# Kernel tuning notes

Measured on AMD Instinct MI355X. Metric: run time of the kernel, lower is better.

Reference implementation:

```python
import jax, jax.numpy as jnp
import numpy as np

N_HEAD = 12
MIN_SIZE = 4
MAX_SIZE = 8
TOP_M = 16
ALPHA = 1.0
EPS = 1e-6
NEG_INF = -1e30


def setup_inputs() -> dict:
    key = jax.random.key(0)
    ks = jax.random.split(key, 4)
    B, T, C = 2, 512, 768
    x = jax.random.normal(ks[0], (B, T, C), jnp.float32)
    w_qkv = jax.random.normal(ks[1], (C, 3 * C), jnp.float32) * (1.0 / np.sqrt(C))
    b_qkv = jnp.zeros((3 * C,), jnp.float32)
    w_proj = jax.random.normal(ks[2], (C, C), jnp.float32) * (1.0 / np.sqrt(C))
    b_proj = jnp.zeros((C,), jnp.float32)
    gate_param = jnp.zeros((), jnp.float32)  # dpp_gate_init = 0.0 -> gate = 0.5
    return {"x": x, "w_qkv": w_qkv, "b_qkv": b_qkv, "w_proj": w_proj,
            "b_proj": b_proj, "gate_param": gate_param}


def _dpp_token(i, q_i, k, v):
    """Greedy DPP subset selection + attention for one query token.
    q_i: [hd], k/v: [T, hd]. Faithful to the torch greedy loop, vectorized
    over candidates with incremental Gram construction (scores only gate the
    discrete selection, so they are computed under stop_gradient, matching
    torch where they only feed Python comparisons)."""
    T, hd = k.shape
    kc = jax.lax.stop_gradient(k)
    qc = jax.lax.stop_gradient(q_i)
    # causal similarity, topk candidates
    sim = jnp.where(jnp.arange(T) <= i, kc @ qc, NEG_INF)
    _, topidx = jax.lax.top_k(sim, TOP_M)  # [M]
    # candidates = top-min(TOP_M, i+1) causal neighbors, excluding i itself
    cand_active = (jnp.arange(TOP_M) < jnp.minimum(TOP_M, i + 1)) & (topidx != i)
    cand_keys = kc[topidx]                              # [M, hd]
    cnorm = jnp.sum(cand_keys * cand_keys, axis=-1)     # [M]

    sel_idx = jnp.zeros((MAX_SIZE,), jnp.int32).at[0].set(i)
    sel_count = jnp.int32(1)
    # initial score: log(det([k_i.k_i]) + eps) / 1**alpha
    cur = jnp.log(jnp.dot(kc[i], kc[i]) + EPS)
    stopped = jnp.bool_(False)
    eye = jnp.eye(MAX_SIZE, dtype=jnp.float32)
    slots = jnp.arange(MAX_SIZE)

    for _ in range(MAX_SIZE - 1):
        rowmask = slots < sel_count                       # [S] current subset rows
        pos = (slots == sel_count).astype(jnp.float32)    # slot for new candidate
        Ksel = kc[sel_idx] * rowmask[:, None].astype(jnp.float32)  # [S, hd]
        G0 = Ksel @ Ksel.T                                # [S, S]
        cross = cand_keys @ Ksel.T                        # [M, S]
        # Gc[c,a,b] = G0[a,b] + pos[a]*cross[c,b] + pos[b]*cross[c,a] + pos[a]pos[b]*cnorm[c]
        Gc = (G0[None]
              + pos[None, :, None] * cross[:, None, :]
              + pos[None, None, :] * cross[:, :, None]
              + (pos[:, None] * pos[None, :])[None] * cnorm[:, None, None])
        newmask = rowmask | (slots == sel_count)
        # identity-pad unused rows/cols so det equals det of the active submatrix
        Gc = Gc + (eye * (1.0 - newmask.astype(jnp.float32)))[None]
        dets = jnp.linalg.det(Gc)                         # [M] (float32, as torch)
        size = (sel_count + 1).astype(jnp.float32)
        score = jnp.log(dets + EPS) / size ** ALPHA       # minimize_det=False
        masked = jnp.where(cand_active, score, NEG_INF)
        best = jnp.argmax(masked)
        best_score = masked[best]
        any_cand = jnp.any(cand_active)
        take = any_cand & (~stopped) & ((best_score > cur) | (sel_count < MIN_SIZE))
        sel_idx = jnp.where(take, sel_idx.at[sel_count].set(topidx[best].astype(jnp.int32)), sel_idx)
        cand_active = jnp.where(take, cand_active.at[best].set(False), cand_active)
        cur = jnp.where(take, best_score, cur)
        sel_count = sel_count + take.astype(jnp.int32)
        stopped = stopped | (~take)

    # attention over the selected subset (gradients flow through k, v, q here)
    rowmask = slots < sel_count
    Ks = k[sel_idx]
    Vs = v[sel_idx]
    logits = jnp.where(rowmask, (Ks @ q_i) / np.float32(np.sqrt(hd)), NEG_INF)
    w = jax.nn.softmax(logits)
    return w @ Vs


def _forward(x, w_qkv, b_qkv, w_proj, b_proj, gate_param):
    B, T, C = x.shape
    hd = C // N_HEAD
    qkv = x @ w_qkv + b_qkv
    q, k, v = jnp.split(qkv, 3, axis=-1)

    def heads(t):  # [B,T,C] -> [B*NH, T, hd]
        return t.reshape(B, T, N_HEAD, hd).transpose(0, 2, 1, 3).reshape(B * N_HEAD, T, hd)

    q, k, v = heads(q), heads(k), heads(v)

    # standard causal softmax attention (flash path, dropout=0 at eval)
    scale = np.float32(1.0 / np.sqrt(hd))
    att = jnp.einsum('nqd,nkd->nqk', q, k) * scale
    causal = jnp.tril(jnp.ones((T, T), bool))
    att = jnp.where(causal[None], att, NEG_INF)
    y_std = jnp.einsum('nqk,nkd->nqd', jax.nn.softmax(att, axis=-1), v)

    # DPP greedy-selection attention, vmapped over tokens and (batch*head)
    dpp_head = jax.vmap(_dpp_token, in_axes=(0, 0, None, None))
    y_dpp = jax.vmap(lambda qh, kh, vh: dpp_head(jnp.arange(T), qh, kh, vh))(q, k, v)

    gate = jax.nn.sigmoid(gate_param)
    y = gate * y_dpp + (1.0 - gate) * y_std
    y = y.reshape(B, N_HEAD, T, hd).transpose(0, 2, 1, 3).reshape(B, T, C)
    return y @ w_proj + b_proj


def reference(x, w_qkv, b_qkv, w_proj, b_proj, gate_param):
    return _forward(x, w_qkv, b_qkv, w_proj, b_proj, gate_param)
```

## Files before the change

kernel.cpp:

```cpp
#include <hip/hip_runtime.h>
#include <math.h>

constexpr int SEQ   = 512;
constexpr int HDIM  = 64;
constexpr int NHEAD = 12;
constexpr int NBATCH = 2;
constexpr int CDIM  = 768;
constexpr int TOPM  = 16;
constexpr int SMAX  = 8;
constexpr float NEGINF = -1e30f;

__device__ inline void gload_lds16(const float* src, float* lds_base)
{
    __builtin_amdgcn_global_load_lds(
        (const __attribute__((address_space(1))) void*)src,
        (__attribute__((address_space(3))) void*)lds_base, 16, 0, 0);
}

__global__ __launch_bounds__(128) void qkv_gemm_kernel(
    const float* __restrict__ x, const float* __restrict__ w,
    float* __restrict__ partial)
{
    __shared__ float As[64 * 32];
    __shared__ float Bs[32 * 64];
    const int bm = blockIdx.y * 64;
    const int bn = blockIdx.x * 64;
    const int kbase = blockIdx.z * 192;
    const int tid = threadIdx.x;
    const int wid = tid >> 6;
    const int tm = (tid >> 4) << 3;
    const int tn = (tid & 15) << 2;
    const int swzA = ((tid >> 4) & 3) << 2;
    float acc[8][4] = {};
    for (int t = 0; t < 6; ++t) {
        const int k0 = kbase + t * 32;
        #pragma unroll
        for (int l = 0; l < 4; ++l) {
            int slot = l * 128 + tid;
            int row = slot >> 3;
            int kq = (slot & 7) << 2;
            int kqs = kq ^ (((row >> 3) & 3) << 2);
            gload_lds16(x + (bm + row) * CDIM + k0 + kqs,
                        As + (l * 128 + wid * 64) * 4);
        }
        #pragma unroll
        for (int l = 0; l < 4; ++l) {
            int slot = l * 128 + tid;
            int kk = slot >> 4;
            int col = (slot & 15) << 2;
            gload_lds16(w + (k0 + kk) * (3 * CDIM) + bn + col,
                        Bs + (l * 128 + wid * 64) * 4);
        }
        __syncthreads();
        #pragma unroll
        for (int k4 = 0; k4 < 8; ++k4) {
            float ar[8][4];
            #pragma unroll
            for (int u = 0; u < 8; ++u) {
                float4 a4 = *(const float4*)(As + (tm + u) * 32 + ((k4 << 2) ^ swzA));
                ar[u][0] = a4.x; ar[u][1] = a4.y;
                ar[u][2] = a4.z; ar[u][3] = a4.w;
            }
            #pragma unroll
            for (int j = 0; j < 4; ++j) {
                float4 b4 = *(const float4*)(Bs + ((k4 << 2) + j) * 64 + tn);
                float bb[4] = {b4.x, b4.y, b4.z, b4.w};
                #pragma unroll
                for (int u = 0; u < 8; ++u)
                    #pragma unroll
                    for (int w2 = 0; w2 < 4; ++w2)
                        acc[u][w2] = fmaf(ar[u][j], bb[w2], acc[u][w2]);
            }
        }
        __syncthreads();
    }
    float* dst = partial + (size_t)blockIdx.z * (1024 * 2304);
    #pragma unroll
    for (int u = 0; u < 8; ++u) {
        float4 o = {acc[u][0], acc[u][1], acc[u][2], acc[u][3]};
        *(float4*)(dst + (size_t)(bm + tm + u) * 2304 + bn + tn) = o;
    }
}

__global__ __launch_bounds__(256) void qkv_reduce_kernel(
    const float* __restrict__ partial, const float* __restrict__ bias,
    float* __restrict__ q, float* __restrict__ k, float* __restrict__ v)
{
    const int idx = blockIdx.x * 256 + threadIdx.x;
    const int m = idx / 576;
    const int cc = (idx - m * 576) << 2;
    const size_t MN = (size_t)1024 * 2304;
    float4 p0 = *(const float4*)(partial + (size_t)m * 2304 + cc);
    float4 p1 = *(const float4*)(partial + MN + (size_t)m * 2304 + cc);
    float4 p2 = *(const float4*)(partial + 2 * MN + (size_t)m * 2304 + cc);
    float4 p3 = *(const float4*)(partial + 3 * MN + (size_t)m * 2304 + cc);
    float4 b4 = *(const float4*)(bias + cc);
    float4 o = {((p0.x + p1.x) + p2.x) + p3.x + b4.x,
                ((p0.y + p1.y) + p2.y) + p3.y + b4.y,
                ((p0.z + p1.z) + p2.z) + p3.z + b4.z,
                ((p0.w + p1.w) + p2.w) + p3.w + b4.w};
    const int part = cc / CDIM;
    const int c2 = cc - part * CDIM;
    const int h = c2 >> 6, d = c2 & 63;
    const int b_ = m >> 9, t = m & 511;
    float* dst = (part == 0) ? q : ((part == 1) ? k : v);
    *(float4*)(dst + ((((size_t)b_ * NHEAD + h) * SEQ) + t) * HDIM + d) = o;
}

__global__ __launch_bounds__(256) void qkkt_kernel(
    const float* __restrict__ q, const float* __restrict__ k,
    float* __restrict__ S, float* __restrict__ KKT)
{
    __shared__ float Qs[64][68];
    __shared__ float Ka[64][68];
    __shared__ float Kb[64][68];
    const int e = blockIdx.x;
    const int n = blockIdx.y;
    int it = 0, start = 0;
    while (start + it + 1 <= e) { start += it + 1; ++it; }
    const int jt = e - start;
    const int tid = threadIdx.x;
    const float* qh = q + (size_t)n * SEQ * HDIM;
    const float* kh = k + (size_t)n * SEQ * HDIM;

    #pragma unroll
    for (int l = 0; l < 4; ++l) {
        int idx = tid + l * 256;
        int tok = idx >> 4, d4 = (idx & 15) << 2;
        *(float4*)&Qs[tok][d4] = *(const float4*)(qh + (it * 64 + tok) * HDIM + d4);
        *(float4*)&Ka[tok][d4] = *(const float4*)(kh + (it * 64 + tok) * HDIM + d4);
        *(float4*)&Kb[tok][d4] = *(const float4*)(kh + (jt * 64 + tok) * HDIM + d4);
    }
    __syncthreads();

    const int tm = (tid >> 4) << 2;
    const int tn = (tid & 15) << 2;
    float sacc[4][4] = {};
    float gacc[4][4] = {};
    #pragma unroll 4
    for (int d4 = 0; d4 < 16; ++d4) {
        float4 qr[4], ar[4], br[4];
        #pragma unroll
        for (int u = 0; u < 4; ++u) {
            qr[u] = *(const float4*)&Qs[tm + u][d4 << 2];
            ar[u] = *(const float4*)&Ka[tm + u][d4 << 2];
        }
        #pragma unroll
        for (int w2 = 0; w2 < 4; ++w2)
            br[w2] = *(const float4*)&Kb[tn + w2][d4 << 2];
        #pragma unroll
        for (int u = 0; u < 4; ++u)
            #pragma unroll
            for (int w2 = 0; w2 < 4; ++w2) {
                float s = sacc[u][w2];
                s = fmaf(qr[u].x, br[w2].x, s);
                s = fmaf(qr[u].y, br[w2].y, s);
                s = fmaf(qr[u].z, br[w2].z, s);
                s = fmaf(qr[u].w, br[w2].w, s);
                sacc[u][w2] = s;
                float g = gacc[u][w2];
                g = fmaf(ar[u].x, br[w2].x, g);
                g = fmaf(ar[u].y, br[w2].y, g);
                g = fmaf(ar[u].z, br[w2].z, g);
                g = fmaf(ar[u].w, br[w2].w, g);
                gacc[u][w2] = g;
            }
    }
    float* gdst = KKT + ((size_t)n * 36 + e) * 4096;
    #pragma unroll
    for (int u = 0; u < 4; ++u) {
        int i = it * 64 + tm + u;
        float4 o = {sacc[u][0], sacc[u][1], sacc[u][2], sacc[u][3]};
        *(float4*)(S + ((size_t)n * SEQ + i) * SEQ + jt * 64 + tn) = o;
        float4 g = {gacc[u][0], gacc[u][1], gacc[u][2], gacc[u][3]};
        *(float4*)(gdst + (tm + u) * 64 + tn) = g;
    }
}

__device__ inline double hybrid_log(double a)
{
    unsigned long long b = __double_as_longlong(a);
    int e2 = (int)((b >> 52) & 0x7FF) - 1022;
    double m = __longlong_as_double((b & 0x000FFFFFFFFFFFFFULL) |
                                    0x3FE0000000000000ULL);
    return ((double)__log2f((float)m) + (double)e2) * 0.6931471805599453;
}

__device__ inline double rsqrt64(double x)
{
    double r = (double)rsqrtf((float)x);
    r = r * (1.5 - 0.5 * x * r * r);
    return r;
}

#define CSW(a, b)                                                        \
    {                                                                    \
        bool sw = (v##a < v##b) || ((v##a == v##b) && (j##a > j##b));    \
        float tf = sw ? v##b : v##a;                                     \
        float uf = sw ? v##a : v##b;                                     \
        int ti = sw ? j##b : j##a;                                       \
        int ui = sw ? j##a : j##b;                                       \
        v##a = tf; v##b = uf; j##a = ti; j##b = ui;                      \
    }

__global__ __launch_bounds__(128) void dpp_kernel(
    const float* __restrict__ v, float* __restrict__ S,
    const float* __restrict__ KKT, const float* __restrict__ gate_p,
    float* __restrict__ y, float* __restrict__ denomArr)
{
    const int tid  = threadIdx.x;
    const int wid  = tid >> 6;
    const int lane = tid & 63;
    const int i = blockIdx.x * 2 + wid;
    const int n = blockIdx.y;
    const float* vh = v + (size_t)n * SEQ * HDIM;
    const float* KKTh = KKT + (size_t)n * 36 * 4096;
    float* Srow = S + ((size_t)n * SEQ + i) * SEQ;

    __shared__ float prow[2][SEQ];
    __shared__ float gramf[2][17][17];
    __shared__ int   eidx[2][17];
    __shared__ int   selS[2][SMAX];

    float sim8[8];
    #pragma unroll
    for (int m = 0; m < 8; ++m) {
        int j = lane + (m << 6);
        sim8[m] = (j <= i) ? Srow[j] : NEGINF;
    }
    if (lane < SMAX) selS[wid][lane] = i;

    {
        float v0 = sim8[0], v1 = sim8[1], v2 = sim8[2], v3 = sim8[3],
              v4 = sim8[4], v5 = sim8[5], v6 = sim8[6], v7 = sim8[7];
        int j0 = lane, j1 = lane + 64, j2 = lane + 128, j3 = lane + 192,
            j4 = lane + 256, j5 = lane + 320, j6 = lane + 384, j7 = lane + 448;
        CSW(0, 1) CSW(2, 3) CSW(4, 5) CSW(6, 7)
        CSW(0, 2) CSW(1, 3) CSW(4, 6) CSW(5, 7)
        CSW(1, 2) CSW(5, 6)
        CSW(0, 4) CSW(1, 5) CSW(2, 6) CSW(3, 7)
        CSW(2, 4) CSW(3, 5)
        CSW(1, 2) CSW(3, 4) CSW(5, 6)

        if (lane == 0) eidx[wid][0] = i;
        #pragma unroll
        for (int s = 0; s < TOPM; ++s) {
            float rv = v0;
            #pragma unroll
            for (int off = 32; off; off >>= 1)
                rv = fmaxf(rv, __shfl_xor(rv, off));
            unsigned long long tied = __ballot(v0 == rv);
            int ri;
            if (__popcll(tied) == 1) {
                ri = __shfl(j0, (int)__builtin_ctzll(tied));
            } else {
                int cnd = (v0 == rv) ? j0 : 0x7FFFFFFF;
                #pragma unroll
                for (int off = 32; off; off >>= 1)
                    cnd = min(cnd, __shfl_xor(cnd, off));
                ri = cnd;
            }
            if (lane == 0) eidx[wid][1 + s] = ri;
            if (v0 == rv && j0 == ri) {
                v0 = v1; j0 = j1; v1 = v2; j1 = j2; v2 = v3; j2 = j3;
                v3 = v4; j3 = j4; v4 = v5; j4 = j5; v5 = v6; j5 = j6;
                v6 = v7; j6 = j7; v7 = -3e38f; j7 = 1023;
            }
        }
    }

    const float scale = 0.125f;
    float lm = -3e38f;
    #pragma unroll
    for (int m = 0; m < 8; ++m) lm = fmaxf(lm, sim8[m]);
    #pragma unroll
    for (int off = 32; off; off >>= 1) lm = fmaxf(lm, __shfl_xor(lm, off));
    const float mx = lm * scale;
    float sum = 0.f;
    #pragma unroll
    for (int m = 0; m < 8; ++m) {
        float p = expf(sim8[m] * scale - mx);
        int j = lane + (m << 6);
        prow[wid][j] = p;
        Srow[j] = p;
        sum += p;
    }
    #pragma unroll
    for (int off = 32; off; off >>= 1) sum += __shfl_xor(sum, off);
    const float denom = sum;
    asm volatile("s_waitcnt lgkmcnt(0)" ::: "memory");

    for (int e = lane; e < 153; e += 64) {
        int a = (int)((sqrtf(8.f * (float)e + 1.f) - 1.f) * 0.5f);
        int st = (a * (a + 1)) >> 1;
        if (st > e) { --a; st = (a * (a + 1)) >> 1; }
        else if (st + a + 1 <= e) { ++a; st = (a * (a + 1)) >> 1; }
        int b = e - st;
        int ra = eidx[wid][a], rb = eidx[wid][b];
        int row = ra > rb ? ra : rb;
        int col = ra > rb ? rb : ra;
        int itt = row >> 6, jtt = col >> 6;
        int p = ((itt * (itt + 1)) >> 1) + jtt;
        float s = KKTh[((size_t)p * 64 + (row & 63)) * 64 + (col & 63)];
        gramf[wid][a][b] = s;
        gramf[wid][b][a] = s;
    }
    asm volatile("s_waitcnt lgkmcnt(0)" ::: "memory");

    int sc = 1;
    {
        const int c = lane;
        const bool isCand = (c < TOPM);
        const int nvalid = (i + 1 < TOPM) ? (i + 1) : TOPM;
        bool active = isCand && (c < nvalid) && (eidx[wid][1 + c] != i);
        double zc[7];
        #pragma unroll
        for (int t = 0; t < 7; ++t) zc[t] = 0.0;
        double det = (double)gramf[wid][0][0];
        double cur = 0.0;
        double invL00 = rsqrt64(det > 0.0 ? det : 1e-30);
        double dcv = 0.0;
        if (isCand) {
            zc[0] = (double)gramf[wid][1 + c][0] * invL00;
            dcv = (double)gramf[wid][1 + c][1 + c] - zc[0] * zc[0];
        }

        for (int it2 = 0; it2 < SMAX - 1; ++it2) {
            double argc = det * dcv + 1e-6;
            double key = active ? (argc > 0.0 ? argc : 1e300) : -1.0;
            int rc = c;
            #pragma unroll
            for (int off = 1; off <= 8; off <<= 1) {
                double ov = __shfl_xor(key, off);
                int    oc = __shfl_xor(rc, off);
                if (ov > key || (ov == key && oc < rc)) { key = ov; rc = oc; }
            }
            rc = __shfl(rc, 0);
            bool any = (__any(active ? 1 : 0) != 0);
            double dbest = __shfl(dcv, rc);
            bool take;
            if (it2 < 2) {
                take = any;
            } else {
                double argb = det * dbest + 1e-6;
                bool pos = argb > 0.0;
                double score = hybrid_log(pos ? argb : 1.0) / (double)(sc + 1);
                take = any && (it2 < 3 || (pos && score > cur));
                if (take) cur = pos ? score : __builtin_nan("");
            }
            if (!take) break;

            double invLss = rsqrt64(dbest > 1e-30 ? dbest : 1e-30);
            double zb[7];
            #pragma unroll
            for (int t = 0; t < 7; ++t) zb[t] = __shfl(zc[t], rc);
            if (isCand) {
                double crossn = (double)gramf[wid][1 + c][1 + rc];
                double s2 = 0.0;
                #pragma unroll
                for (int t = 0; t < 7; ++t) s2 += zc[t] * zb[t];
                double znew = (crossn - s2) * invLss;
                #pragma unroll
                for (int t = 0; t < 7; ++t) if (t == sc) zc[t] = znew;
                dcv -= znew * znew;
            }
            det = det * dbest;
            if (c == rc) active = false;
            if (lane == 0) selS[wid][sc] = eidx[wid][1 + rc];
            ++sc;
        }
    }

    int selI[SMAX];
    #pragma unroll
    for (int s = 0; s < SMAX; ++s) selI[s] = selS[wid][s];
    float wsum = 0.f;
    #pragma unroll
    for (int s = 0; s < SMAX; ++s) if (s < sc) wsum += prow[wid][selI[s]];
    float yd = 0.f;
    #pragma unroll
    for (int s = 0; s < SMAX; ++s)
        if (s < sc) yd = fmaf(prow[wid][selI[s]], vh[selI[s] * HDIM + lane], yd);
    const float gp = gate_p[0];
    const float gate = 1.f / (1.f + expf(-gp));
    y[((size_t)n * SEQ + i) * HDIM + lane] = gate * yd / wsum;
    if (lane == 0) denomArr[n * SEQ + i] = denom;
}

__global__ __launch_bounds__(256) void pv_gemm_kernel(
    const float* __restrict__ P, const float* __restrict__ v,
    const float* __restrict__ denomArr, const float* __restrict__ gate_p,
    float* __restrict__ y)
{
    __shared__ float Ps[32][36];
    __shared__ float Vs[32][68];
    const int tt = blockIdx.x;
    const int n  = blockIdx.y;
    const int t0 = tt * 32;
    const int tid = threadIdx.x;
    const float* Ph = P + (size_t)n * SEQ * SEQ;
    const float* vh = v + (size_t)n * SEQ * HDIM;
    const int tm = (tid >> 4) << 1;
    const int tn = (tid & 15) << 2;
    float acc[2][4] = {};
    const int jmax = t0 + 32;
    for (int j0 = 0; j0 < jmax; j0 += 32) {
        {
            int tok = tid >> 3, j4 = (tid & 7) << 2;
            *(float4*)&Ps[tok][j4] =
                *(const float4*)(Ph + (t0 + tok) * SEQ + j0 + j4);
        }
        #pragma unroll
        for (int l = 0; l < 2; ++l) {
            int idx = tid + l * 256;
            int j = idx >> 4, d4 = (idx & 15) << 2;
            *(float4*)&Vs[j][d4] = *(const float4*)(vh + (j0 + j) * HDIM + d4);
        }
        __syncthreads();
        #pragma unroll
        for (int j4 = 0; j4 < 8; ++j4) {
            float4 p0r = *(const float4*)&Ps[tm + 0][j4 << 2];
            float4 p1r = *(const float4*)&Ps[tm + 1][j4 << 2];
            float pr[2][4] = {{p0r.x, p0r.y, p0r.z, p0r.w},
                              {p1r.x, p1r.y, p1r.z, p1r.w}};
            #pragma unroll
            for (int l = 0; l < 4; ++l) {
                float4 v4 = *(const float4*)&Vs[(j4 << 2) + l][tn];
                float vv[4] = {v4.x, v4.y, v4.z, v4.w};
                #pragma unroll
                for (int u = 0; u < 2; ++u)
                    #pragma unroll
                    for (int w2 = 0; w2 < 4; ++w2)
                        acc[u][w2] = fmaf(pr[u][l], vv[w2], acc[u][w2]);
            }
        }
        __syncthreads();
    }
    const float gp = gate_p[0];
    const float gate = 1.f / (1.f + expf(-gp));
    #pragma unroll
    for (int u = 0; u < 2; ++u) {
        int i = t0 + tm + u;
        float den = denomArr[n * SEQ + i];
        #pragma unroll
        for (int w2 = 0; w2 < 4; ++w2) {
            int d = tn + w2;
            size_t off = ((size_t)n * SEQ + i) * HDIM + d;
            y[off] += (1.f - gate) * acc[u][w2] / den;
        }
    }
}

__global__ __launch_bounds__(256) void proj_gemm_kernel(
    const float* __restrict__ y, const float* __restrict__ w,
    float* __restrict__ partial)
{
    __shared__ float As[128][36];
    __shared__ float Bs[32][68];
    const int bm = blockIdx.y * 128;
    const int bn = blockIdx.x * 64;
    const int kbase = blockIdx.z * 96;
    const int tid = threadIdx.x;
    const int tm = (tid >> 4) << 3;
    const int tn = (tid & 15) << 2;
    const int blk = tid >> 3;
    const int bln = (tid & 7) << 3;

    float acc[8][4] = {};
    for (int t = 0; t < 3; ++t) {
        const int k0 = kbase + t * 32;
        float4 av[4];
        #pragma unroll
        for (int l = 0; l < 4; ++l) {
            int idx = tid + l * 256;
            int row = bm + (idx >> 3);
            int col = k0 + ((idx & 7) << 2);
            int b_ = row >> 9, tk = row & 511;
            int h = col >> 6, d = col & 63;
            av[l] = *(const float4*)(y + ((((size_t)b_ * NHEAD + h) * SEQ) + tk) * HDIM + d);
        }
        float4 b0 = *(const float4*)(w + (k0 + blk) * CDIM + bn + bln);
        float4 b1 = *(const float4*)(w + (k0 + blk) * CDIM + bn + bln + 4);
        #pragma unroll
        for (int l = 0; l < 4; ++l) {
            int idx = tid + l * 256;
            int row = idx >> 3, kq = (idx & 7) << 2;
            *(float4*)&As[row][kq] = av[l];
        }
        *(float4*)&Bs[blk][bln] = b0;
        *(float4*)&Bs[blk][bln + 4] = b1;
        __syncthreads();
        #pragma unroll
        for (int k4 = 0; k4 < 8; ++k4) {
            float ar[8][4];
            #pragma unroll
            for (int u = 0; u < 8; ++u) {
                float4 a4 = *(const float4*)&As[tm + u][k4 << 2];
                ar[u][0] = a4.x; ar[u][1] = a4.y;
                ar[u][2] = a4.z; ar[u][3] = a4.w;
            }
            #pragma unroll
            for (int j = 0; j < 4; ++j) {
                float4 b4 = *(const float4*)&Bs[(k4 << 2) + j][tn];
                float bb[4] = {b4.x, b4.y, b4.z, b4.w};
                #pragma unroll
                for (int u = 0; u < 8; ++u)
                    #pragma unroll
                    for (int w2 = 0; w2 < 4; ++w2)
                        acc[u][w2] = fmaf(ar[u][j], bb[w2], acc[u][w2]);
            }
        }
        __syncthreads();
    }
    float* dst = partial + (size_t)blockIdx.z * (1024 * 768);
    #pragma unroll
    for (int u = 0; u < 8; ++u) {
        float4 o = {acc[u][0], acc[u][1], acc[u][2], acc[u][3]};
        *(float4*)(dst + (size_t)(bm + tm + u) * 768 + bn + tn) = o;
    }
}

__global__ __launch_bounds__(256) void proj_reduce_kernel(
    const float* __restrict__ partial, const float* __restrict__ bias,
    float* __restrict__ out)
{
    const int idx = blockIdx.x * 256 + threadIdx.x;
    const int m = idx / 192;
    const int cc = (idx - m * 192) << 2;
    const size_t MN = (size_t)1024 * 768;
    float4 s = *(const float4*)(partial + (size_t)m * 768 + cc);
    #pragma unroll
    for (int z = 1; z < 8; ++z) {
        float4 p = *(const float4*)(partial + (size_t)z * MN + (size_t)m * 768 + cc);
        s.x += p.x; s.y += p.y; s.z += p.z; s.w += p.w;
    }
    float4 b4 = *(const float4*)(bias + cc);
    float4 o = {s.x + b4.x, s.y + b4.y, s.z + b4.z, s.w + b4.w};
    *(float4*)(out + (size_t)m * 768 + cc) = o;
}

extern "C" void kernel_launch(void* const* d_in, const int* in_sizes, int n_in,
                              void* d_out, int out_size, void* d_ws, size_t ws_size,
                              hipStream_t stream)
{
    const float* x      = (const float*)d_in[0];
    const float* w_qkv  = (const float*)d_in[1];
    const float* b_qkv  = (const float*)d_in[2];
    const float* w_proj = (const float*)d_in[3];
    const float* b_proj = (const float*)d_in[4];
    const float* gate_p = (const float*)d_in[5];
    float* out = (float*)d_out;

    float* ws = (float*)d_ws;
    const size_t HS = (size_t)NBATCH * NHEAD * SEQ * HDIM;
    const size_t SS = (size_t)NBATCH * NHEAD * SEQ * SEQ;
    float* q   = ws;
    float* k   = q + HS;
    float* v   = k + HS;
    float* y   = v + HS;
    float* S   = y + HS;
    float* den = S + SS;
    float* KKT = den + 16384;

    qkv_gemm_kernel<<<dim3((3 * CDIM) / 64, (NBATCH * SEQ) / 64, 4), 128, 0, stream>>>(
        x, w_qkv, S);
    qkv_reduce_kernel<<<2304, 256, 0, stream>>>(S, b_qkv, q, k, v);
    qkkt_kernel<<<dim3(36, NBATCH * NHEAD), 256, 0, stream>>>(q, k, S, KKT);
    dpp_kernel<<<dim3(SEQ / 2, NBATCH * NHEAD), 128, 0, stream>>>(
        v, S, KKT, gate_p, y, den);
    pv_gemm_kernel<<<dim3(SEQ / 32, NBATCH * NHEAD), 256, 0, stream>>>(
        S, v, den, gate_p, y);
    proj_gemm_kernel<<<dim3(CDIM / 64, (NBATCH * SEQ) / 128, 8), 256, 0, stream>>>(
        y, w_proj, S);
    proj_reduce_kernel<<<768, 256, 0, stream>>>(S, b_proj, out);
}
```

Baseline: 182.9 us.

## Compute QKV projection with split-bf16 MFMA emulating fp32 precision

Replaces the fp32 FMA split-K GEMM and its separate reduce kernel for the QKV projection with a bf16x3 split scheme on MFMA matrix cores. Inputs and weights are split into high, mid and low bf16 parts, with the weights transposed in a preprocessing kernel. Six MFMA products recover near-fp32 accuracy, and bias plus the head-scatter are fused into the epilogue. The goal is to cut FMA-bound GEMM time and the partial-sum round trip. In exchange it adds two conversion kernels, and the weight split is redone on every call.

```diff
diff --git a/kernel.cpp b/kernel.cpp
--- a/kernel.cpp
+++ b/kernel.cpp
@@ -10,101 +10,174 @@
 constexpr int SMAX  = 8;
 constexpr float NEGINF = -1e30f;
 
-__device__ inline void gload_lds16(const float* src, float* lds_base)
+typedef short bf16x8 __attribute__((ext_vector_type(8)));
+typedef float f32x4  __attribute__((ext_vector_type(4)));
+
+__device__ inline void gload_lds16(const void* src, void* lds_base)
 {
     __builtin_amdgcn_global_load_lds(
         (const __attribute__((address_space(1))) void*)src,
         (__attribute__((address_space(3))) void*)lds_base, 16, 0, 0);
 }
 
-__global__ __launch_bounds__(128) void qkv_gemm_kernel(
-    const float* __restrict__ x, const float* __restrict__ w,
-    float* __restrict__ partial)
-{
-    __shared__ float As[64 * 32];
-    __shared__ float Bs[32 * 64];
+__device__ inline unsigned short f2bf(float f)
+{
+    unsigned u = __float_as_uint(f);
+    return (unsigned short)((u + 0x7FFFu + ((u >> 16) & 1u)) >> 16);
+}
+__device__ inline float bf2f(unsigned short h)
+{
+    return __uint_as_float((unsigned)h << 16);
+}
+
+__global__ __launch_bounds__(256) void split_x_kernel(
+    const float* __restrict__ x, unsigned short* __restrict__ xh,
+    unsigned short* __restrict__ xm, unsigned short* __restrict__ xl)
+{
+    const int idx = (blockIdx.x * 256 + threadIdx.x) * 4;
+    float4 v = *(const float4*)(x + idx);
+    float vv[4] = {v.x, v.y, v.z, v.w};
+    unsigned short h[4], m[4], l[4];
+    #pragma unroll
+    for (int e = 0; e < 4; ++e) {
+        float f = vv[e];
+        unsigned short bh = f2bf(f);
+        float r1 = f - bf2f(bh);
+        unsigned short bm2 = f2bf(r1);
+        float r2 = r1 - bf2f(bm2);
+        h[e] = bh; m[e] = bm2; l[e] = f2bf(r2);
+    }
+    *(ushort4*)(xh + idx) = make_ushort4(h[0], h[1], h[2], h[3]);
+    *(ushort4*)(xm + idx) = make_ushort4(m[0], m[1], m[2], m[3]);
+    *(ushort4*)(xl + idx) = make_ushort4(l[0], l[1], l[2], l[3]);
+}
+
+__global__ __launch_bounds__(256) void tsplit_w_kernel(
+    const float* __restrict__ w, unsigned short* __restrict__ wh,
+    unsigned short* __restrict__ wm, unsigned short* __restrict__ wl)
+{
+    __shared__ float T[64][65];
+    const int c0 = blockIdx.x * 64;
+    const int k0 = blockIdx.y * 64;
+    const int tid = threadIdx.x;
+    #pragma unroll
+    for (int i = 0; i < 16; ++i) {
+        int idx = tid + i * 256;
+        int kk = idx >> 6, cc = idx & 63;
+        T[kk][cc] = w[(size_t)(k0 + kk) * (3 * CDIM) + c0 + cc];
+    }
+    __syncthreads();
+    #pragma unroll
+    for (int i = 0; i < 16; ++i) {
+        int idx = tid + i * 256;
+        int col = idx >> 6, kk = idx & 63;
+        float f = T[kk][col];
+        unsigned short bh = f2bf(f);
+        float r1 = f - bf2f(bh);
+        unsigned short bm2 = f2bf(r1);
+        float r2 = r1 - bf2f(bm2);
+        size_t o = (size_t)(c0 + col) * CDIM + k0 + kk;
+        wh[o] = bh; wm[o] = bm2; wl[o] = f2bf(r2);
+    }
+}
+
+__global__ __launch_bounds__(64) void qkv_mfma_kernel(
+    const unsigned short* __restrict__ xh, const unsigned short* __restrict__ xm,
+    const unsigned short* __restrict__ xl, const unsigned short* __restrict__ wh,
+    const unsigned short* __restrict__ wm, const unsigned short* __restrict__ wl,
+    const float* __restrict__ bias,
+    float* __restrict__ q, float* __restrict__ k, float* __restrict__ v)
+{
+    __shared__ unsigned short As[3][64 * 32];
+    __shared__ unsigned short Bs[3][64 * 32];
+    const int bn = blockIdx.x * 64;
     const int bm = blockIdx.y * 64;
-    const int bn = blockIdx.x * 64;
-    const int kbase = blockIdx.z * 192;
     const int tid = threadIdx.x;
-    const int wid = tid >> 6;
-    const int tm = (tid >> 4) << 3;
-    const int tn = (tid & 15) << 2;
-    const int swzA = ((tid >> 4) & 3) << 2;
-    float acc[8][4] = {};
-    for (int t = 0; t < 6; ++t) {
-        const int k0 = kbase + t * 32;
-        #pragma unroll
-        for (int l = 0; l < 4; ++l) {
-            int slot = l * 128 + tid;
-            int row = slot >> 3;
-            int kq = (slot & 7) << 2;
-            int kqs = kq ^ (((row >> 3) & 3) << 2);
-            gload_lds16(x + (bm + row) * CDIM + k0 + kqs,
-                        As + (l * 128 + wid * 64) * 4);
-        }
-        #pragma unroll
-        for (int l = 0; l < 4; ++l) {
-            int slot = l * 128 + tid;
-            int kk = slot >> 4;
-            int col = (slot & 15) << 2;
-            gload_lds16(w + (k0 + kk) * (3 * CDIM) + bn + col,
-                        Bs + (l * 128 + wid * 64) * 4);
+    const int lrow = tid & 15;
+    const int lk8 = (tid >> 4) << 3;
+
+    f32x4 acc[4][4];
+    #pragma unroll
+    for (int a = 0; a < 4; ++a)
+        #pragma unroll
+        for (int b = 0; b < 4; ++b)
+            acc[a][b] = (f32x4){0.f, 0.f, 0.f, 0.f};
+
+    const unsigned short* xs[3] = {xh, xm, xl};
+    const unsigned short* wsrc[3] = {wh, wm, wl};
+
+    for (int k0 = 0; k0 < CDIM; k0 += 32) {
+        #pragma unroll
+        for (int c = 0; c < 3; ++c) {
+            #pragma unroll
+            for (int l = 0; l < 4; ++l) {
+                int slot = l * 64 + tid;
+                int row = slot >> 2;
+                int k8 = (slot & 3) << 3;
+                gload_lds16(xs[c] + (size_t)(bm + row) * CDIM + k0 + k8,
+                            &As[c][l * 512]);
+            }
+        }
+        #pragma unroll
+        for (int c = 0; c < 3; ++c) {
+            #pragma unroll
+            for (int l = 0; l < 4; ++l) {
+                int slot = l * 64 + tid;
+                int col = slot >> 2;
+                int k8 = (slot & 3) << 3;
+                gload_lds16(wsrc[c] + (size_t)(bn + col) * CDIM + k0 + k8,
+                            &Bs[c][l * 512]);
+            }
         }
         __syncthreads();
-        #pragma unroll
-        for (int k4 = 0; k4 < 8; ++k4) {
-            float ar[8][4];
-            #pragma unroll
-            for (int u = 0; u < 8; ++u) {
-                float4 a4 = *(const float4*)(As + (tm + u) * 32 + ((k4 << 2) ^ swzA));
-                ar[u][0] = a4.x; ar[u][1] = a4.y;
-                ar[u][2] = a4.z; ar[u][3] = a4.w;
-            }
-            #pragma unroll
-            for (int j = 0; j < 4; ++j) {
-                float4 b4 = *(const float4*)(Bs + ((k4 << 2) + j) * 64 + tn);
-                float bb[4] = {b4.x, b4.y, b4.z, b4.w};
-                #pragma unroll
-                for (int u = 0; u < 8; ++u)
-                    #pragma unroll
-                    for (int w2 = 0; w2 < 4; ++w2)
-                        acc[u][w2] = fmaf(ar[u][j], bb[w2], acc[u][w2]);
+
+        bf16x8 bf[3][4];
+        #pragma unroll
+        for (int c = 0; c < 3; ++c)
+            #pragma unroll
+            for (int ni = 0; ni < 4; ++ni)
+                bf[c][ni] = *(const bf16x8*)&Bs[c][(ni * 16 + lrow) * 32 + lk8];
+
+        #pragma unroll
+        for (int mi = 0; mi < 4; ++mi) {
+            bf16x8 ah = *(const bf16x8*)&As[0][(mi * 16 + lrow) * 32 + lk8];
+            bf16x8 am = *(const bf16x8*)&As[1][(mi * 16 + lrow) * 32 + lk8];
+            bf16x8 al = *(const bf16x8*)&As[2][(mi * 16 + lrow) * 32 + lk8];
+            #pragma unroll
+            for (int ni = 0; ni < 4; ++ni) {
+                f32x4 a = acc[mi][ni];
+                a = __builtin_amdgcn_mfma_f32_16x16x32_bf16(al, bf[0][ni], a, 0, 0, 0);
+                a = __builtin_amdgcn_mfma_f32_16x16x32_bf16(ah, bf[2][ni], a, 0, 0, 0);
+                a = __builtin_amdgcn_mfma_f32_16x16x32_bf16(am, bf[1][ni], a, 0, 0, 0);
+                a = __builtin_amdgcn_mfma_f32_16x16x32_bf16(am, bf[0][ni], a, 0, 0, 0);
+                a = __builtin_amdgcn_mfma_f32_16x16x32_bf16(ah, bf[1][ni], a, 0, 0, 0);
+                a = __builtin_amdgcn_mfma_f32_16x16x32_bf16(ah, bf[0][ni], a, 0, 0, 0);
+                acc[mi][ni] = a;
             }
         }
         __syncthreads();
     }
-    float* dst = partial + (size_t)blockIdx.z * (1024 * 2304);
-    #pragma unroll
-    for (int u = 0; u < 8; ++u) {
-        float4 o = {acc[u][0], acc[u][1], acc[u][2], acc[u][3]};
-        *(float4*)(dst + (size_t)(bm + tm + u) * 2304 + bn + tn) = o;
-    }
-}
-
-__global__ __launch_bounds__(256) void qkv_reduce_kernel(
-    const float* __restrict__ partial, const float* __restrict__ bias,
-    float* __restrict__ q, float* __restrict__ k, float* __restrict__ v)
-{
-    const int idx = blockIdx.x * 256 + threadIdx.x;
-    const int m = idx / 576;
-    const int cc = (idx - m * 576) << 2;
-    const size_t MN = (size_t)1024 * 2304;
-    float4 p0 = *(const float4*)(partial + (size_t)m * 2304 + cc);
-    float4 p1 = *(const float4*)(partial + MN + (size_t)m * 2304 + cc);
-    float4 p2 = *(const float4*)(partial + 2 * MN + (size_t)m * 2304 + cc);
-    float4 p3 = *(const float4*)(partial + 3 * MN + (size_t)m * 2304 + cc);
-    float4 b4 = *(const float4*)(bias + cc);
-    float4 o = {((p0.x + p1.x) + p2.x) + p3.x + b4.x,
-                ((p0.y + p1.y) + p2.y) + p3.y + b4.y,
-                ((p0.z + p1.z) + p2.z) + p3.z + b4.z,
-                ((p0.w + p1.w) + p2.w) + p3.w + b4.w};
-    const int part = cc / CDIM;
-    const int c2 = cc - part * CDIM;
-    const int h = c2 >> 6, d = c2 & 63;
-    const int b_ = m >> 9, t = m & 511;
-    float* dst = (part == 0) ? q : ((part == 1) ? k : v);
-    *(float4*)(dst + ((((size_t)b_ * NHEAD + h) * SEQ) + t) * HDIM + d) = o;
+
+    const int rbase = (tid >> 4) << 2;
+    #pragma unroll
+    for (int mi = 0; mi < 4; ++mi) {
+        #pragma unroll
+        for (int ni = 0; ni < 4; ++ni) {
+            int cc = bn + ni * 16 + lrow;
+            float bval = bias[cc];
+            int part = cc / CDIM;
+            int c2 = cc - part * CDIM;
+            int hh = c2 >> 6, d = c2 & 63;
+            float* dst = (part == 0) ? q : ((part == 1) ? k : v);
+            #pragma unroll
+            for (int r = 0; r < 4; ++r) {
+                int m = bm + mi * 16 + rbase + r;
+                int b_ = m >> 9, t = m & 511;
+                dst[((((size_t)b_ * NHEAD + hh) * SEQ) + t) * HDIM + d] =
+                    acc[mi][ni][r] + bval;
+            }
+        }
+    }
 }
 
 __global__ __launch_bounds__(256) void qkkt_kernel(
@@ -562,9 +635,18 @@
     float* den = S + SS;
     float* KKT = den + 16384;
 
-    qkv_gemm_kernel<<<dim3((3 * CDIM) / 64, (NBATCH * SEQ) / 64, 4), 128, 0, stream>>>(
-        x, w_qkv, S);
-    qkv_reduce_kernel<<<2304, 256, 0, stream>>>(S, b_qkv, q, k, v);
+    unsigned short* us = (unsigned short*)S;
+    unsigned short* xh = us;
+    unsigned short* xm = us + 786432;
+    unsigned short* xl = us + 1572864;
+    unsigned short* wh = us + 2359296;
+    unsigned short* wm = us + 2359296 + 1769472;
+    unsigned short* wl = us + 2359296 + 3538944;
+
+    split_x_kernel<<<768, 256, 0, stream>>>(x, xh, xm, xl);
+    tsplit_w_kernel<<<dim3(36, 12), 256, 0, stream>>>(w_qkv, wh, wm, wl);
+    qkv_mfma_kernel<<<dim3(36, 16), 64, 0, stream>>>(
+        xh, xm, xl, wh, wm, wl, b_qkv, q, k, v);
     qkkt_kernel<<<dim3(36, NBATCH * NHEAD), 256, 0, stream>>>(q, k, S, KKT);
     dpp_kernel<<<dim3(SEQ / 2, NBATCH * NHEAD), 128, 0, stream>>>(
         v, S, KKT, gate_p, y, den);
```

New measurement: 177.6 us. 2.9% less time.
